# Kernel tuning notes

Measured on AMD Instinct MI355X. Metric: run time of the kernel, lower is better.

The kernel has to match this reference:

```python
import jax, jax.numpy as jnp
import numpy as np

B, N, C, H, P = 8, 4096, 256, 4, 64  # batch, tokens, hidden, heads, proj_size


def setup_inputs() -> dict:
    key = jax.random.key(0)
    ks = jax.random.split(key, 6)
    sc = 0.02
    x = jax.random.normal(ks[0], (B, N, C), jnp.float32)
    bank = jax.random.normal(ks[1], (B, N, C), jnp.float32)  # unused by forward, kept for fidelity
    W_qkvv = jax.random.normal(ks[2], (4 * C, C), jnp.float32) * sc  # Linear(C, 4C), no bias
    W_E = jax.random.normal(ks[3], (P, N), jnp.float32) * sc          # E = F shared Linear(N, P)
    b_E = jnp.zeros((P,), jnp.float32)
    temperature = jnp.ones((H, 1, 1), jnp.float32)
    temperature2 = jnp.ones((H, 1, 1), jnp.float32)
    W_out1 = jax.random.normal(ks[4], (C // 2, C), jnp.float32) * sc  # out_proj (spatial branch)
    b_out1 = jnp.zeros((C // 2,), jnp.float32)
    W_out2 = jax.random.normal(ks[5], (C // 2, C), jnp.float32) * sc  # out_proj2 (channel branch)
    b_out2 = jnp.zeros((C // 2,), jnp.float32)
    prelu_a = jnp.array(0.25, jnp.float32)  # nn.PReLU() default: single shared slope
    return {"x": x, "bank": bank, "W_qkvv": W_qkvv, "W_E": W_E, "b_E": b_E,
            "temperature": temperature, "temperature2": temperature2,
            "W_out1": W_out1, "b_out1": b_out1, "W_out2": W_out2, "b_out2": b_out2,
            "prelu_a": prelu_a}


def _l2norm(t):
    # torch F.normalize(dim=-1): x / max(||x||_2, eps)
    return t / jnp.maximum(jnp.linalg.norm(t, axis=-1, keepdims=True), 1e-12)


def reference(x, bank, W_qkvv, W_E, b_E, temperature, temperature2,
              W_out1, b_out1, W_out2, b_out2, prelu_a):
    Bb, Nn, Cc = x.shape
    Hh = temperature.shape[0]
    d = Cc // Hh
    # qkvv projection -> [4, B, H, N, d], then transpose token/feature axes -> [B, H, d, N]
    qkvv = (x @ W_qkvv.T).reshape(Bb, Nn, 4, Hh, d).transpose(2, 0, 3, 1, 4)
    q, k, v_ca, v_sa = (qkvv[0].transpose(0, 1, 3, 2), qkvv[1].transpose(0, 1, 3, 2),
                        qkvv[2].transpose(0, 1, 3, 2), qkvv[3].transpose(0, 1, 3, 2))
    # shared linear E=F projects the token axis N -> P (applied to UNnormalized k, v_sa)
    k_proj = jnp.einsum('bhdn,pn->bhdp', k, W_E) + b_E      # [B,H,d,P]
    v_sa_proj = jnp.einsum('bhdn,pn->bhdp', v_sa, W_E) + b_E  # [B,H,d,P]
    qn = _l2norm(q)
    kn = _l2norm(k)
    # channel attention: [B,H,d,d]
    attn_ca = jax.nn.softmax(jnp.einsum('bhdn,bhen->bhde', qn, kn) * temperature, axis=-1)
    x_ca = jnp.einsum('bhde,bhen->bhdn', attn_ca, v_ca).transpose(0, 3, 1, 2).reshape(Bb, Nn, Cc)
    # spatial attention (projected): [B,H,N,P]
    attn_sa = jax.nn.softmax(jnp.einsum('bhdn,bhdp->bhnp', qn, k_proj) * temperature2, axis=-1)
    x_sa = jnp.einsum('bhnp,bhdp->bhnd', attn_sa, v_sa_proj).transpose(0, 2, 1, 3).reshape(Bb, Nn, Cc)
    x_sa = x_sa @ W_out1.T + b_out1
    x_ca = x_ca @ W_out2.T + b_out2
    out = jnp.concatenate([x_sa, x_ca], axis=-1)
    return jnp.where(out >= 0, out, prelu_a * out)  # PReLU
```

## Files before the change

### kernel.cpp

```cpp
#include <hip/hip_runtime.h>
#include <cstdint>
#include <cstddef>

constexpr int B_ = 8, N_ = 4096, C_ = 256, H_ = 4, D_ = 64, P_ = 64;
constexpr int OC_ = 4 * C_;
constexpr int M_  = B_ * N_;
constexpr int GX_ROWS = 320;
constexpr int KS_G = 8;
constexpr int XT_TILES = M_ / 64;

#define DEV_INLINE __device__ __forceinline__

typedef unsigned short ushort_t;
typedef __attribute__((ext_vector_type(8))) short short8;
typedef __attribute__((ext_vector_type(4))) short short4v;
typedef __attribute__((ext_vector_type(4))) float floatx4;

DEV_INLINE short f2bf(float f) {
  unsigned int u = __builtin_bit_cast(unsigned int, f);
  u += 0x7FFFu + ((u >> 16) & 1u);
  return (short)(u >> 16);
}
DEV_INLINE float bf2f(ushort_t u) {
  return __builtin_bit_cast(float, (unsigned int)u << 16);
}
DEV_INLINE short4v cvt4(float4 v) {
  short4v s = {f2bf(v.x), f2bf(v.y), f2bf(v.z), f2bf(v.w)};
  return s;
}

__global__ __launch_bounds__(256) void k_cast(const float* __restrict__ x,
                                              const float* __restrict__ Wq,
                                              const float* __restrict__ WE,
                                              const float* __restrict__ W1,
                                              const float* __restrict__ W2,
                                              ushort_t* __restrict__ xb,
                                              ushort_t* __restrict__ xt,
                                              ushort_t* __restrict__ wqb,
                                              ushort_t* __restrict__ web,
                                              ushort_t* __restrict__ w1b,
                                              ushort_t* __restrict__ w2b) {
  const int t = threadIdx.x;
  if (blockIdx.x >= XT_TILES) {
    constexpr size_t WQ4 = (size_t)OC_ * C_ / 4;
    constexpr size_t WE4 = (size_t)P_ * N_ / 4;
    constexpr size_t W14 = (size_t)128 * C_ / 4;
    constexpr size_t TOTW4 = WQ4 + WE4 + 2 * W14;
    const size_t stride = (size_t)128 * 256;
    for (size_t i = (size_t)(blockIdx.x - XT_TILES) * 256 + t; i < TOTW4; i += stride) {
      const float* src; ushort_t* dst; size_t o;
      if (i < WQ4) { src = Wq; dst = wqb; o = i; }
      else if (i < WQ4 + WE4) { src = WE; dst = web; o = i - WQ4; }
      else if (i < WQ4 + WE4 + W14) { src = W1; dst = w1b; o = i - WQ4 - WE4; }
      else { src = W2; dst = w2b; o = i - WQ4 - WE4 - W14; }
      float4 v = ((const float4*)src)[o];
      *(short4v*)&dst[o * 4] = cvt4(v);
    }
    return;
  }
  __shared__ __align__(16) short Xs[64 * 264];
  const int n0 = blockIdx.x * 64;
  const int b = n0 >> 12, nl = n0 & 4095;
#pragma unroll
  for (int rep = 0; rep < 16; ++rep) {
    const int f4 = rep * 256 + t;
    const int row = f4 >> 6, c4 = f4 & 63;
    float4 v = *(const float4*)&x[(size_t)(n0 + row) * 256 + c4 * 4];
    short4v s = cvt4(v);
    *(short4v*)&xb[(size_t)(n0 + row) * 256 + c4 * 4] = s;
    *(short4v*)&Xs[row * 264 + c4 * 4] = s;
  }
  __syncthreads();
  const int ch = t;
  ushort_t* dst = &xt[((size_t)b * 256 + ch) * 4096 + nl];
#pragma unroll
  for (int g = 0; g < 8; ++g) {
    short8 o;
#pragma unroll
    for (int i = 0; i < 8; ++i) o[i] = Xs[(g * 8 + i) * 264 + ch];
    *(short8*)&dst[g * 8] = o;
  }
}

__global__ __launch_bounds__(512) void k_qv(const ushort_t* __restrict__ xb,
                                            const ushort_t* __restrict__ wqb,
                                            ushort_t* __restrict__ qv) {
  __shared__ __align__(16) short As[128 * 72];
  __shared__ __align__(16) short Bs[256 * 72];
  const int bm = blockIdx.x * 128;
  const int y = blockIdx.y;
  const int wrow = y ? 512 : 0;
  const int t = threadIdx.x;
  const int oc = t & 7, rr = t >> 3;
  const int lane = t & 63, wave = t >> 6;
  const int m16 = lane & 15, quad = lane >> 4;
  const int wm = (wave >> 2) << 6, wn = (wave & 3) << 6;
  floatx4 acc[4][4];
#pragma unroll
  for (int i = 0; i < 4; ++i)
#pragma unroll
    for (int j = 0; j < 4; ++j) acc[i][j] = (floatx4)(0.f);
#pragma unroll 1
  for (int k0 = 0; k0 < 256; k0 += 64) {
    short8 a8[2], b8[4];
#pragma unroll
    for (int rp = 0; rp < 2; ++rp)
      a8[rp] = *(const short8*)&xb[(size_t)(bm + rr + 64 * rp) * 256 + k0 + 8 * oc];
#pragma unroll
    for (int rp = 0; rp < 4; ++rp)
      b8[rp] = *(const short8*)&wqb[(size_t)(wrow + rr + 64 * rp) * 256 + k0 + 8 * oc];
    __syncthreads();
#pragma unroll
    for (int rp = 0; rp < 2; ++rp)
      *(short8*)&As[(rr + 64 * rp) * 72 + 8 * oc] = a8[rp];
#pragma unroll
    for (int rp = 0; rp < 4; ++rp)
      *(short8*)&Bs[(rr + 64 * rp) * 72 + 8 * oc] = b8[rp];
    __syncthreads();
#pragma unroll
    for (int ks = 0; ks < 2; ++ks) {
      short8 af[4], bf[4];
#pragma unroll
      for (int i = 0; i < 4; ++i)
        af[i] = *(const short8*)&As[(wm + i * 16 + m16) * 72 + ks * 32 + quad * 8];
#pragma unroll
      for (int j = 0; j < 4; ++j)
        bf[j] = *(const short8*)&Bs[(wn + j * 16 + m16) * 72 + ks * 32 + quad * 8];
#pragma unroll
      for (int i = 0; i < 4; ++i)
#pragma unroll
        for (int j = 0; j < 4; ++j)
          acc[i][j] = __builtin_amdgcn_mfma_f32_16x16x32_bf16(af[i], bf[j], acc[i][j], 0, 0, 0);
    }
  }
#pragma unroll
  for (int i = 0; i < 4; ++i)
#pragma unroll
    for (int r = 0; r < 4; ++r) {
      const int gr = bm + wm + i * 16 + quad * 4 + r;
#pragma unroll
      for (int j = 0; j < 4; ++j)
        qv[(size_t)gr * 512 + y * 256 + wn + j * 16 + m16] =
            (ushort_t)f2bf(acc[i][j][r]);
    }
}

__global__ __launch_bounds__(512) void k_gram(const ushort_t* __restrict__ xt,
                                              const ushort_t* __restrict__ web,
                                              float* __restrict__ Gxp) {
  __shared__ __align__(16) short As[128 * 72];
  __shared__ __align__(16) short Bs[256 * 72];
  const int job = blockIdx.x;
  const int y = blockIdx.y;
  const int b = y >> 3, ksp = y & 7;
  const int t = threadIdx.x;
  const int oc = t & 7, rr = t >> 3;
  const int lane = t & 63, wave = t >> 6;
  const int m16 = lane & 15, quad = lane >> 4;
  const int wm = (wave >> 2) << 6, wn = (wave & 3) << 6;
  const ushort_t* Asrc = (job < 2)
      ? xt + (size_t)(b * 256 + job * 128) * 4096 : web;
  const ushort_t* Bsrc = xt + (size_t)b * 256 * 4096;
  floatx4 acc[4][4];
#pragma unroll
  for (int i = 0; i < 4; ++i)
#pragma unroll
    for (int j = 0; j < 4; ++j) acc[i][j] = (floatx4)(0.f);
#pragma unroll 1
  for (int it = 0; it < 8; ++it) {
    const int n0 = ksp * 512 + it * 64;
    short8 a8[2], b8[4];
#pragma unroll
    for (int rp = 0; rp < 2; ++rp) {
      int ar = rr + 64 * rp;
      if (job == 2) ar &= 63;
      a8[rp] = *(const short8*)&Asrc[(size_t)ar * 4096 + n0 + 8 * oc];
    }
#pragma unroll
    for (int rp = 0; rp < 4; ++rp)
      b8[rp] = *(const short8*)&Bsrc[(size_t)(rr + 64 * rp) * 4096 + n0 + 8 * oc];
    __syncthreads();
#pragma unroll
    for (int rp = 0; rp < 2; ++rp)
      *(short8*)&As[(rr + 64 * rp) * 72 + 8 * oc] = a8[rp];
#pragma unroll
    for (int rp = 0; rp < 4; ++rp)
      *(short8*)&Bs[(rr + 64 * rp) * 72 + 8 * oc] = b8[rp];
    __syncthreads();
#pragma unroll
    for (int ks = 0; ks < 2; ++ks) {
      if (job < 2) {
        short8 af[4], bf[4];
#pragma unroll
        for (int i = 0; i < 4; ++i)
          af[i] = *(const short8*)&As[(wm + i * 16 + m16) * 72 + ks * 32 + quad * 8];
#pragma unroll
        for (int j = 0; j < 4; ++j)
          bf[j] = *(const short8*)&Bs[(wn + j * 16 + m16) * 72 + ks * 32 + quad * 8];
#pragma unroll
        for (int i = 0; i < 4; ++i)
#pragma unroll
          for (int j = 0; j < 4; ++j)
            acc[i][j] = __builtin_amdgcn_mfma_f32_16x16x32_bf16(af[i], bf[j], acc[i][j], 0, 0, 0);
      } else {
        short8 af[4], bf[2];
#pragma unroll
        for (int i = 0; i < 4; ++i)
          af[i] = *(const short8*)&As[(i * 16 + m16) * 72 + ks * 32 + quad * 8];
#pragma unroll
        for (int j = 0; j < 2; ++j)
          bf[j] = *(const short8*)&Bs[(wave * 32 + j * 16 + m16) * 72 + ks * 32 + quad * 8];
#pragma unroll
        for (int i = 0; i < 4; ++i)
#pragma unroll
          for (int j = 0; j < 2; ++j)
            acc[i][j] = __builtin_amdgcn_mfma_f32_16x16x32_bf16(af[i], bf[j], acc[i][j], 0, 0, 0);
      }
    }
  }
  float* pb = Gxp + (size_t)y * (GX_ROWS * 256);
  if (job < 2) {
#pragma unroll
    for (int i = 0; i < 4; ++i)
#pragma unroll
      for (int r = 0; r < 4; ++r) {
        const int grow = job * 128 + wm + i * 16 + quad * 4 + r;
#pragma unroll
        for (int j = 0; j < 4; ++j)
          pb[(size_t)grow * 256 + wn + j * 16 + m16] = acc[i][j][r];
      }
  } else {
#pragma unroll
    for (int i = 0; i < 4; ++i)
#pragma unroll
      for (int r = 0; r < 4; ++r) {
        const int grow = 256 + i * 16 + quad * 4 + r;
#pragma unroll
        for (int j = 0; j < 2; ++j)
          pb[(size_t)grow * 256 + wave * 32 + j * 16 + m16] = acc[i][j][r];
      }
  }
}

__global__ __launch_bounds__(256) void k_gred(const float* __restrict__ Gxp,
                                              float* __restrict__ Gx) {
  const int i = blockIdx.x * 256 + threadIdx.x;
  constexpr int PB4 = GX_ROWS * 256 / 4;
  const int fb = i / PB4, rem = i - fb * PB4;
  const float4* p = (const float4*)Gxp;
  float4 s = p[(size_t)fb * KS_G * PB4 + rem];
#pragma unroll
  for (int k = 1; k < KS_G; ++k) {
    float4 v = p[((size_t)fb * KS_G + k) * PB4 + rem];
    s.x += v.x; s.y += v.y; s.z += v.z; s.w += v.w;
  }
  ((float4*)Gx)[i] = s;
}

__global__ __launch_bounds__(256) void k_mid1(const ushort_t* __restrict__ wqb,
                                              const float* __restrict__ Gx,
                                              ushort_t* __restrict__ T2b,
                                              float* __restrict__ ssq) {
  __shared__ __align__(16) short As[128 * 72];
  __shared__ __align__(16) short Bs[128 * 72];
  const int bm = blockIdx.x * 128;
  const int b  = blockIdx.y >> 1;
  const int jb = blockIdx.y & 1;
  const int t = threadIdx.x;
  const int oc = t & 7;
  const int rr = t >> 3;
  const int lane = t & 63, wave = t >> 6;
  const int m16 = lane & 15, quad = lane >> 4;
  const int wm = (wave >> 1) << 6, wn = (wave & 1) << 6;
  const float* Bsrc = Gx + ((size_t)b * GX_ROWS + jb * 128) * 256;
  floatx4 acc[4][4];
#pragma unroll
  for (int i = 0; i < 4; ++i)
#pragma unroll
    for (int j = 0; j < 4; ++j) acc[i][j] = (floatx4)(0.f);
#pragma unroll 1
  for (int k0 = 0; k0 < 256; k0 += 64) {
    short8 a8[4], b8[4];
#pragma unroll
    for (int j = 0; j < 4; ++j) {
      const int r = rr + 32 * j;
      a8[j] = *(const short8*)&wqb[(size_t)(bm + r) * 256 + k0 + 8 * oc];
      float4 g0 = *(const float4*)&Bsrc[(size_t)r * 256 + k0 + 8 * oc];
      float4 g1 = *(const float4*)&Bsrc[(size_t)r * 256 + k0 + 8 * oc + 4];
      short8 bb;
      bb[0] = f2bf(g0.x); bb[1] = f2bf(g0.y); bb[2] = f2bf(g0.z); bb[3] = f2bf(g0.w);
      bb[4] = f2bf(g1.x); bb[5] = f2bf(g1.y); bb[6] = f2bf(g1.z); bb[7] = f2bf(g1.w);
      b8[j] = bb;
    }
    __syncthreads();
#pragma unroll
    for (int j = 0; j < 4; ++j) {
      const int r = rr + 32 * j;
      *(short8*)&As[r * 72 + 8 * oc] = a8[j];
      *(short8*)&Bs[r * 72 + 8 * oc] = b8[j];
    }
    __syncthreads();
#pragma unroll
    for (int ks = 0; ks < 2; ++ks) {
      short8 af[4], bf[4];
#pragma unroll
      for (int i = 0; i < 4; ++i)
        af[i] = *(const short8*)&As[(wm + i * 16 + m16) * 72 + ks * 32 + quad * 8];
#pragma unroll
      for (int j = 0; j < 4; ++j)
        bf[j] = *(const short8*)&Bs[(wn + j * 16 + m16) * 72 + ks * 32 + quad * 8];
#pragma unroll
      for (int i = 0; i < 4; ++i)
#pragma unroll
        for (int j = 0; j < 4; ++j)
          acc[i][j] = __builtin_amdgcn_mfma_f32_16x16x32_bf16(af[i], bf[j], acc[i][j], 0, 0, 0);
    }
  }
#pragma unroll
  for (int i = 0; i < 4; ++i)
#pragma unroll
    for (int r = 0; r < 4; ++r) {
      const int gr = bm + wm + i * 16 + quad * 4 + r;
      float s = 0.f;
#pragma unroll
      for (int j = 0; j < 4; ++j) {
        const int col = jb * 128 + wn + j * 16 + m16;
        T2b[((size_t)b * 512 + gr) * 256 + col] = (ushort_t)f2bf(acc[i][j][r]);
        s += bf2f(wqb[(size_t)gr * 256 + col]) * acc[i][j][r];
      }
      s += __shfl_xor(s, 1);
      s += __shfl_xor(s, 2);
      s += __shfl_xor(s, 4);
      s += __shfl_xor(s, 8);
      if (m16 == 0) atomicAdd(&ssq[b * 512 + gr], s);
    }
}

__global__ __launch_bounds__(256) void k_mid2(const ushort_t* __restrict__ wqb,
                                              const ushort_t* __restrict__ T2b,
                                              const float* __restrict__ Gx,
                                              const float* __restrict__ ssq,
                                              const float* __restrict__ bE,
                                              const float* __restrict__ t1,
                                              const float* __restrict__ t2,
                                              ushort_t* __restrict__ ab,
                                              ushort_t* __restrict__ ksb,
                                              ushort_t* __restrict__ vsb) {
  const int bh = blockIdx.x;
  const int job = blockIdx.y;
  const int b = bh >> 2, h = bh & 3;
  const int wave = threadIdx.x >> 6;
  const int lane = threadIdx.x & 63;
  const int m16 = lane & 15, quad = lane >> 4;
  const int Abase = (job == 0 ? 0 : (job == 1 ? 256 : 768)) + h * 64;
  const int arow = Abase + 16 * wave + m16;
  floatx4 acc[4];
#pragma unroll
  for (int j = 0; j < 4; ++j) acc[j] = (floatx4)(0.f);
#pragma unroll
  for (int ks = 0; ks < 8; ++ks) {
    const int boct = ks * 32 + quad * 8;
    short8 af = *(const short8*)&wqb[(size_t)arow * 256 + boct];
    short8 bf[4];
    if (job == 0) {
#pragma unroll
      for (int j = 0; j < 4; ++j)
        bf[j] = *(const short8*)&T2b[((size_t)b * 512 + 256 + h * 64 + 16 * j + m16) * 256 + boct];
    } else {
#pragma unroll
      for (int j = 0; j < 4; ++j) {
        const float* gp = Gx + ((size_t)b * GX_ROWS + 256 + 16 * j + m16) * 256 + boct;
        float4 g0 = *(const float4*)gp;
        float4 g1 = *(const float4*)(gp + 4);
        short8 bb;
        bb[0] = f2bf(g0.x); bb[1] = f2bf(g0.y); bb[2] = f2bf(g0.z); bb[3] = f2bf(g0.w);
        bb[4] = f2bf(g1.x); bb[5] = f2bf(g1.y); bb[6] = f2bf(g1.z); bb[7] = f2bf(g1.w);
        bf[j] = bb;
      }
    }
#pragma unroll
    for (int j = 0; j < 4; ++j)
      acc[j] = __builtin_amdgcn_mfma_f32_16x16x32_bf16(af, bf[j], acc[j], 0, 0, 0);
  }
  if (job == 0) {
    const float t1h = t1[h];
    float rnk[4];
#pragma unroll
    for (int j = 0; j < 4; ++j)
      rnk[j] = 1.f / fmaxf(sqrtf(ssq[b * 512 + 256 + h * 64 + 16 * j + m16]), 1e-12f);
#pragma unroll
    for (int r = 0; r < 4; ++r) {
      const int d = 16 * wave + quad * 4 + r;
      const float rq = 1.f / fmaxf(sqrtf(ssq[b * 512 + h * 64 + d]), 1e-12f);
      float l[4];
      float m = -1e30f;
#pragma unroll
      for (int j = 0; j < 4; ++j) {
        l[j] = acc[j][r] * rq * rnk[j] * t1h;
        m = fmaxf(m, l[j]);
      }
      m = fmaxf(m, __shfl_xor(m, 1));
      m = fmaxf(m, __shfl_xor(m, 2));
      m = fmaxf(m, __shfl_xor(m, 4));
      m = fmaxf(m, __shfl_xor(m, 8));
      float s = 0.f;
#pragma unroll
      for (int j = 0; j < 4; ++j) {
        l[j] = __expf(l[j] - m);
        s += l[j];
      }
      s += __shfl_xor(s, 1);
      s += __shfl_xor(s, 2);
      s += __shfl_xor(s, 4);
      s += __shfl_xor(s, 8);
      const float inv = 1.f / s;
#pragma unroll
      for (int j = 0; j < 4; ++j)
        ab[(size_t)bh * 4096 + d * 64 + 16 * j + m16] = (ushort_t)f2bf(l[j] * inv);
    }
  } else if (job == 1) {
    const float tt = t2[h];
#pragma unroll
    for (int r = 0; r < 4; ++r) {
      const int d = 16 * wave + quad * 4 + r;
      const float rq = 1.f / fmaxf(sqrtf(ssq[b * 512 + h * 64 + d]), 1e-12f);
#pragma unroll
      for (int j = 0; j < 4; ++j) {
        const int p = 16 * j + m16;
        ksb[(size_t)bh * 4096 + p * 64 + d] =
            (ushort_t)f2bf((acc[j][r] + bE[p]) * rq * tt);
      }
    }
  } else {
#pragma unroll
    for (int r = 0; r < 4; ++r) {
      const int d = 16 * wave + quad * 4 + r;
#pragma unroll
      for (int j = 0; j < 4; ++j) {
        const int p = 16 * j + m16;
        vsb[(size_t)bh * 4096 + d * 64 + p] = (ushort_t)f2bf(acc[j][r] + bE[p]);
      }
    }
  }
}

__global__ __launch_bounds__(256) void k_attn(const ushort_t* __restrict__ qv,
                                              const ushort_t* __restrict__ ab,
                                              const ushort_t* __restrict__ ksb,
                                              const ushort_t* __restrict__ vsb,
                                              ushort_t* __restrict__ x_ca,
                                              ushort_t* __restrict__ x_sa) {
  __shared__ float Pl[64][68];
  const int bh = blockIdx.x;
  const int b = bh >> 2, h = bh & 3;
  const int lane = threadIdx.x & 63, wave = threadIdx.x >> 6;
  const int m16 = lane & 15, quad = lane >> 4;
  if (blockIdx.y < 32) {
    const int n0 = blockIdx.y * 128;
    const ushort_t* abb = ab + (size_t)bh * 4096;
    short8 bf[2][4];
#pragma unroll
    for (int ks = 0; ks < 2; ++ks)
#pragma unroll
      for (int j = 0; j < 4; ++j)
        bf[ks][j] = *(const short8*)&abb[(16 * j + m16) * 64 + ks * 32 + quad * 8];
#pragma unroll
    for (int mm = 0; mm < 2; ++mm) {
      const int tokbase = n0 + 64 * mm + 16 * wave;
      const ushort_t* vrow =
          qv + (size_t)(b * N_ + tokbase + m16) * 512 + 256 + h * 64 + quad * 8;
      short8 af0 = *(const short8*)&vrow[0];
      short8 af1 = *(const short8*)&vrow[32];
      floatx4 o[4];
#pragma unroll
      for (int j = 0; j < 4; ++j) o[j] = (floatx4)(0.f);
#pragma unroll
      for (int j = 0; j < 4; ++j) {
        o[j] = __builtin_amdgcn_mfma_f32_16x16x32_bf16(af0, bf[0][j], o[j], 0, 0, 0);
        o[j] = __builtin_amdgcn_mfma_f32_16x16x32_bf16(af1, bf[1][j], o[j], 0, 0, 0);
      }
#pragma unroll
      for (int j = 0; j < 4; ++j)
#pragma unroll
        for (int r = 0; r < 4; ++r)
          x_ca[(size_t)(b * N_ + tokbase + quad * 4 + r) * C_ + h * 64 + 16 * j + m16] =
              (ushort_t)f2bf(o[j][r]);
    }
    return;
  }
  const int n0 = (blockIdx.y - 32) * 64;
  const ushort_t* qrow =
      qv + (size_t)(b * N_ + n0 + 16 * wave + m16) * 512 + h * 64 + quad * 8;
  short8 qf0 = *(const short8*)&qrow[0];
  short8 qf1 = *(const short8*)&qrow[32];
  const ushort_t* kb = ksb + (size_t)bh * 4096;
  const ushort_t* vb = vsb + (size_t)bh * 4096;
  short8 kf[2][4], vf[2][4];
#pragma unroll
  for (int ks = 0; ks < 2; ++ks)
#pragma unroll
    for (int j = 0; j < 4; ++j) {
      kf[ks][j] = *(const short8*)&kb[(16 * j + m16) * 64 + ks * 32 + quad * 8];
      vf[ks][j] = *(const short8*)&vb[(16 * j + m16) * 64 + ks * 32 + quad * 8];
    }
  floatx4 s[4];
#pragma unroll
  for (int j = 0; j < 4; ++j) s[j] = (floatx4)(0.f);
#pragma unroll
  for (int j = 0; j < 4; ++j) {
    s[j] = __builtin_amdgcn_mfma_f32_16x16x32_bf16(qf0, kf[0][j], s[j], 0, 0, 0);
    s[j] = __builtin_amdgcn_mfma_f32_16x16x32_bf16(qf1, kf[1][j], s[j], 0, 0, 0);
  }
  float p[4][4];
#pragma unroll
  for (int r = 0; r < 4; ++r) {
    float mr = fmaxf(fmaxf(s[0][r], s[1][r]), fmaxf(s[2][r], s[3][r]));
    mr = fmaxf(mr, __shfl_xor(mr, 1));
    mr = fmaxf(mr, __shfl_xor(mr, 2));
    mr = fmaxf(mr, __shfl_xor(mr, 4));
    mr = fmaxf(mr, __shfl_xor(mr, 8));
    float sr = 0.f;
#pragma unroll
    for (int j = 0; j < 4; ++j) {
      const float e = __expf(s[j][r] - mr);
      p[j][r] = e;
      sr += e;
    }
    sr += __shfl_xor(sr, 1);
    sr += __shfl_xor(sr, 2);
    sr += __shfl_xor(sr, 4);
    sr += __shfl_xor(sr, 8);
    const float inv = 1.f / sr;
#pragma unroll
    for (int j = 0; j < 4; ++j) p[j][r] *= inv;
  }
#pragma unroll
  for (int j = 0; j < 4; ++j)
#pragma unroll
    for (int r = 0; r < 4; ++r)
      Pl[16 * wave + quad * 4 + r][16 * j + m16] = p[j][r];
  __syncthreads();
  short8 pf[2];
#pragma unroll
  for (int ks = 0; ks < 2; ++ks) {
    float4 x0 = *(const float4*)&Pl[16 * wave + m16][ks * 32 + quad * 8];
    float4 x1 = *(const float4*)&Pl[16 * wave + m16][ks * 32 + quad * 8 + 4];
    short8 v;
    v[0] = f2bf(x0.x); v[1] = f2bf(x0.y); v[2] = f2bf(x0.z); v[3] = f2bf(x0.w);
    v[4] = f2bf(x1.x); v[5] = f2bf(x1.y); v[6] = f2bf(x1.z); v[7] = f2bf(x1.w);
    pf[ks] = v;
  }
  floatx4 o[4];
#pragma unroll
  for (int j = 0; j < 4; ++j) o[j] = (floatx4)(0.f);
#pragma unroll
  for (int j = 0; j < 4; ++j) {
    o[j] = __builtin_amdgcn_mfma_f32_16x16x32_bf16(pf[0], vf[0][j], o[j], 0, 0, 0);
    o[j] = __builtin_amdgcn_mfma_f32_16x16x32_bf16(pf[1], vf[1][j], o[j], 0, 0, 0);
  }
#pragma unroll
  for (int j = 0; j < 4; ++j)
#pragma unroll
    for (int r = 0; r < 4; ++r)
      x_sa[(size_t)(b * N_ + n0 + 16 * wave + quad * 4 + r) * C_ + h * 64 + 16 * j + m16] =
          (ushort_t)f2bf(o[j][r]);
}

__global__ __launch_bounds__(256) void k_out_mfma(const ushort_t* __restrict__ xsa,
                                                  const ushort_t* __restrict__ xca,
                                                  const ushort_t* __restrict__ w1b,
                                                  const float* __restrict__ b1,
                                                  const ushort_t* __restrict__ w2b,
                                                  const float* __restrict__ b2,
                                                  const float* __restrict__ pa,
                                                  float* __restrict__ out) {
  __shared__ __align__(16) short As[128 * 72];
  __shared__ __align__(16) short Bs[128 * 72];
  const int bm = blockIdx.x * 128;
  const int half = blockIdx.y;
  const ushort_t* A = half ? xca : xsa;
  const ushort_t* W = half ? w2b : w1b;
  const float* bias = half ? b2 : b1;
  const int t = threadIdx.x;
  const int oc = t & 7;
  const int rr = t >> 3;
  const int lane = t & 63, wave = t >> 6;
  const int m16 = lane & 15, quad = lane >> 4;
  const int wm = (wave >> 1) << 6, wn = (wave & 1) << 6;
  floatx4 acc[4][4];
#pragma unroll
  for (int i = 0; i < 4; ++i)
#pragma unroll
    for (int j = 0; j < 4; ++j) acc[i][j] = (floatx4)(0.f);
#pragma unroll 1
  for (int k0 = 0; k0 < 256; k0 += 64) {
    short8 a8[4], b8[4];
#pragma unroll
    for (int j = 0; j < 4; ++j) {
      const int r = rr + 32 * j;
      a8[j] = *(const short8*)&A[(size_t)(bm + r) * 256 + k0 + 8 * oc];
      b8[j] = *(const short8*)&W[(size_t)r * 256 + k0 + 8 * oc];
    }
    __syncthreads();
#pragma unroll
    for (int j = 0; j < 4; ++j) {
      const int r = rr + 32 * j;
      *(short8*)&As[r * 72 + 8 * oc] = a8[j];
      *(short8*)&Bs[r * 72 + 8 * oc] = b8[j];
    }
    __syncthreads();
#pragma unroll
    for (int ks = 0; ks < 2; ++ks) {
      short8 af[4], bf[4];
#pragma unroll
      for (int i = 0; i < 4; ++i)
        af[i] = *(const short8*)&As[(wm + i * 16 + m16) * 72 + ks * 32 + quad * 8];
#pragma unroll
      for (int j = 0; j < 4; ++j)
        bf[j] = *(const short8*)&Bs[(wn + j * 16 + m16) * 72 + ks * 32 + quad * 8];
#pragma unroll
      for (int i = 0; i < 4; ++i)
#pragma unroll
        for (int j = 0; j < 4; ++j)
          acc[i][j] = __builtin_amdgcn_mfma_f32_16x16x32_bf16(af[i], bf[j], acc[i][j], 0, 0, 0);
    }
  }
  const float slope = pa[0];
  float bj[4];
#pragma unroll
  for (int j = 0; j < 4; ++j) bj[j] = bias[wn + j * 16 + m16];
#pragma unroll
  for (int i = 0; i < 4; ++i)
#pragma unroll
    for (int r = 0; r < 4; ++r) {
      const int gr = bm + wm + i * 16 + quad * 4 + r;
#pragma unroll
      for (int j = 0; j < 4; ++j) {
        float v = acc[i][j][r] + bj[j];
        v = v >= 0.f ? v : slope * v;
        out[(size_t)gr * C_ + half * 128 + wn + j * 16 + m16] = v;
      }
    }
}

extern "C" void kernel_launch(void* const* d_in, const int* in_sizes, int n_in,
                              void* d_out, int out_size, void* d_ws, size_t ws_size,
                              hipStream_t stream) {
  (void)in_sizes; (void)n_in; (void)out_size; (void)ws_size;
  const float* x  = (const float*)d_in[0];
  const float* Wq = (const float*)d_in[2];
  const float* WE = (const float*)d_in[3];
  const float* bE = (const float*)d_in[4];
  const float* t1 = (const float*)d_in[5];
  const float* t2 = (const float*)d_in[6];
  const float* W1 = (const float*)d_in[7];
  const float* b1 = (const float*)d_in[8];
  const float* W2 = (const float*)d_in[9];
  const float* b2 = (const float*)d_in[10];
  const float* pa = (const float*)d_in[11];
  float* out = (float*)d_out;

  float* ws = (float*)d_ws;
  size_t off = 0;
  float* Gx  = ws + off; off += (size_t)B_ * GX_ROWS * 256;
  float* ssq = ws + off; off += (size_t)B_ * 512;
  float* Gxp = ws + off; off += (size_t)KS_G * B_ * GX_ROWS * 256;
  ushort_t* qv  = (ushort_t*)(ws + off); off += (size_t)M_ * 512 / 2;
  ushort_t* xsa = (ushort_t*)(ws + off); off += (size_t)M_ * C_ / 2;
  ushort_t* xca = (ushort_t*)(ws + off); off += (size_t)M_ * C_ / 2;
  ushort_t* ksb = (ushort_t*)(ws + off); off += 32 * 4096 / 2;
  ushort_t* vsb = (ushort_t*)(ws + off); off += 32 * 4096 / 2;
  ushort_t* ab  = (ushort_t*)(ws + off); off += 32 * 4096 / 2;
  ushort_t* xb  = (ushort_t*)(ws + off); off += (size_t)M_ * C_ / 2;
  ushort_t* xt  = (ushort_t*)(ws + off); off += (size_t)M_ * C_ / 2;
  ushort_t* wqb = (ushort_t*)(ws + off); off += (size_t)OC_ * C_ / 2;
  ushort_t* w1b = (ushort_t*)(ws + off); off += (size_t)128 * C_ / 2;
  ushort_t* w2b = (ushort_t*)(ws + off); off += (size_t)128 * C_ / 2;
  ushort_t* web = (ushort_t*)(ws + off); off += (size_t)P_ * N_ / 2;
  ushort_t* T2b = (ushort_t*)(ws + off); off += (size_t)B_ * 512 * C_ / 2;

  hipMemsetAsync(ssq, 0, (size_t)B_ * 512 * sizeof(float), stream);

  k_cast<<<XT_TILES + 128, 256, 0, stream>>>(x, Wq, WE, W1, W2,
                                             xb, xt, wqb, web, w1b, w2b);
  k_qv<<<dim3(M_ / 128, 2), 512, 0, stream>>>(xb, wqb, qv);
  k_gram<<<dim3(3, B_ * KS_G), 512, 0, stream>>>(xt, web, Gxp);
  k_gred<<<GX_ROWS * 256 * B_ / 4 / 256, 256, 0, stream>>>(Gxp, Gx);
  k_mid1<<<dim3(4, B_ * 2), 256, 0, stream>>>(wqb, Gx, T2b, ssq);
  k_mid2<<<dim3(32, 3), 256, 0, stream>>>(wqb, T2b, Gx, ssq, bE, t1, t2, ab, ksb, vsb);
  k_attn<<<dim3(32, 96), 256, 0, stream>>>(qv, ab, ksb, vsb, xca, xsa);
  k_out_mfma<<<dim3(M_ / 128, 2), 256, 0, stream>>>(xsa, xca, w1b, b1, w2b, b2, pa, out);
}
```

Measured before the change: 237.6 us.

## Fuse q/v projection, attention and output projection into one per-token-tile kernel

Replaces the separate q/v projection GEMM, the attention kernel and the output projection kernel with a single kernel that works on 64-token tiles. It converts x to bf16 in shared memory, computes q and v_ca for all heads, applies spatial softmax attention and channel attention per head (one wave per head), then runs both output projections with PReLU directly from LDS. This removes the global round trips for qv, x_sa, x_ca and xb and two launches. In exchange each block uses about 100KB of LDS and reads weight fragments straight from global/L2 without staging, which may limit occupancy and reload weights once per tile.

```diff
diff --git a/kernel.cpp b/kernel.cpp
--- a/kernel.cpp
+++ b/kernel.cpp
@@ -34,7 +34,6 @@
                                               const float* __restrict__ WE,
                                               const float* __restrict__ W1,
                                               const float* __restrict__ W2,
-                                              ushort_t* __restrict__ xb,
                                               ushort_t* __restrict__ xt,
                                               ushort_t* __restrict__ wqb,
                                               ushort_t* __restrict__ web,
@@ -66,9 +65,7 @@
     const int f4 = rep * 256 + t;
     const int row = f4 >> 6, c4 = f4 & 63;
     float4 v = *(const float4*)&x[(size_t)(n0 + row) * 256 + c4 * 4];
-    short4v s = cvt4(v);
-    *(short4v*)&xb[(size_t)(n0 + row) * 256 + c4 * 4] = s;
-    *(short4v*)&Xs[row * 264 + c4 * 4] = s;
+    *(short4v*)&Xs[row * 264 + c4 * 4] = cvt4(v);
   }
   __syncthreads();
   const int ch = t;
@@ -80,69 +77,6 @@
     for (int i = 0; i < 8; ++i) o[i] = Xs[(g * 8 + i) * 264 + ch];
     *(short8*)&dst[g * 8] = o;
   }
-}
-
-__global__ __launch_bounds__(512) void k_qv(const ushort_t* __restrict__ xb,
-                                            const ushort_t* __restrict__ wqb,
-                                            ushort_t* __restrict__ qv) {
-  __shared__ __align__(16) short As[128 * 72];
-  __shared__ __align__(16) short Bs[256 * 72];
-  const int bm = blockIdx.x * 128;
-  const int y = blockIdx.y;
-  const int wrow = y ? 512 : 0;
-  const int t = threadIdx.x;
-  const int oc = t & 7, rr = t >> 3;
-  const int lane = t & 63, wave = t >> 6;
-  const int m16 = lane & 15, quad = lane >> 4;
-  const int wm = (wave >> 2) << 6, wn = (wave & 3) << 6;
-  floatx4 acc[4][4];
-#pragma unroll
-  for (int i = 0; i < 4; ++i)
-#pragma unroll
-    for (int j = 0; j < 4; ++j) acc[i][j] = (floatx4)(0.f);
-#pragma unroll 1
-  for (int k0 = 0; k0 < 256; k0 += 64) {
-    short8 a8[2], b8[4];
-#pragma unroll
-    for (int rp = 0; rp < 2; ++rp)
-      a8[rp] = *(const short8*)&xb[(size_t)(bm + rr + 64 * rp) * 256 + k0 + 8 * oc];
-#pragma unroll
-    for (int rp = 0; rp < 4; ++rp)
-      b8[rp] = *(const short8*)&wqb[(size_t)(wrow + rr + 64 * rp) * 256 + k0 + 8 * oc];
-    __syncthreads();
-#pragma unroll
-    for (int rp = 0; rp < 2; ++rp)
-      *(short8*)&As[(rr + 64 * rp) * 72 + 8 * oc] = a8[rp];
-#pragma unroll
-    for (int rp = 0; rp < 4; ++rp)
-      *(short8*)&Bs[(rr + 64 * rp) * 72 + 8 * oc] = b8[rp];
-    __syncthreads();
-#pragma unroll
-    for (int ks = 0; ks < 2; ++ks) {
-      short8 af[4], bf[4];
-#pragma unroll
-      for (int i = 0; i < 4; ++i)
-        af[i] = *(const short8*)&As[(wm + i * 16 + m16) * 72 + ks * 32 + quad * 8];
-#pragma unroll
-      for (int j = 0; j < 4; ++j)
-        bf[j] = *(const short8*)&Bs[(wn + j * 16 + m16) * 72 + ks * 32 + quad * 8];
-#pragma unroll
-      for (int i = 0; i < 4; ++i)
-#pragma unroll
-        for (int j = 0; j < 4; ++j)
-          acc[i][j] = __builtin_amdgcn_mfma_f32_16x16x32_bf16(af[i], bf[j], acc[i][j], 0, 0, 0);
-    }
-  }
-#pragma unroll
-  for (int i = 0; i < 4; ++i)
-#pragma unroll
-    for (int r = 0; r < 4; ++r) {
-      const int gr = bm + wm + i * 16 + quad * 4 + r;
-#pragma unroll
-      for (int j = 0; j < 4; ++j)
-        qv[(size_t)gr * 512 + y * 256 + wn + j * 16 + m16] =
-            (ushort_t)f2bf(acc[i][j][r]);
-    }
 }
 
 __global__ __launch_bounds__(512) void k_gram(const ushort_t* __restrict__ xt,
@@ -444,203 +378,230 @@
   }
 }
 
-__global__ __launch_bounds__(256) void k_attn(const ushort_t* __restrict__ qv,
-                                              const ushort_t* __restrict__ ab,
-                                              const ushort_t* __restrict__ ksb,
-                                              const ushort_t* __restrict__ vsb,
-                                              ushort_t* __restrict__ x_ca,
-                                              ushort_t* __restrict__ x_sa) {
-  __shared__ float Pl[64][68];
-  const int bh = blockIdx.x;
-  const int b = bh >> 2, h = bh & 3;
-  const int lane = threadIdx.x & 63, wave = threadIdx.x >> 6;
-  const int m16 = lane & 15, quad = lane >> 4;
-  if (blockIdx.y < 32) {
-    const int n0 = blockIdx.y * 128;
-    const ushort_t* abb = ab + (size_t)bh * 4096;
-    short8 bf[2][4];
-#pragma unroll
-    for (int ks = 0; ks < 2; ++ks)
-#pragma unroll
-      for (int j = 0; j < 4; ++j)
-        bf[ks][j] = *(const short8*)&abb[(16 * j + m16) * 64 + ks * 32 + quad * 8];
-#pragma unroll
-    for (int mm = 0; mm < 2; ++mm) {
-      const int tokbase = n0 + 64 * mm + 16 * wave;
-      const ushort_t* vrow =
-          qv + (size_t)(b * N_ + tokbase + m16) * 512 + 256 + h * 64 + quad * 8;
-      short8 af0 = *(const short8*)&vrow[0];
-      short8 af1 = *(const short8*)&vrow[32];
-      floatx4 o[4];
-#pragma unroll
-      for (int j = 0; j < 4; ++j) o[j] = (floatx4)(0.f);
-#pragma unroll
-      for (int j = 0; j < 4; ++j) {
-        o[j] = __builtin_amdgcn_mfma_f32_16x16x32_bf16(af0, bf[0][j], o[j], 0, 0, 0);
-        o[j] = __builtin_amdgcn_mfma_f32_16x16x32_bf16(af1, bf[1][j], o[j], 0, 0, 0);
-      }
-#pragma unroll
-      for (int j = 0; j < 4; ++j)
-#pragma unroll
-        for (int r = 0; r < 4; ++r)
-          x_ca[(size_t)(b * N_ + tokbase + quad * 4 + r) * C_ + h * 64 + 16 * j + m16] =
-              (ushort_t)f2bf(o[j][r]);
-    }
-    return;
-  }
-  const int n0 = (blockIdx.y - 32) * 64;
-  const ushort_t* qrow =
-      qv + (size_t)(b * N_ + n0 + 16 * wave + m16) * 512 + h * 64 + quad * 8;
-  short8 qf0 = *(const short8*)&qrow[0];
-  short8 qf1 = *(const short8*)&qrow[32];
-  const ushort_t* kb = ksb + (size_t)bh * 4096;
-  const ushort_t* vb = vsb + (size_t)bh * 4096;
-  short8 kf[2][4], vf[2][4];
-#pragma unroll
-  for (int ks = 0; ks < 2; ++ks)
-#pragma unroll
-    for (int j = 0; j < 4; ++j) {
-      kf[ks][j] = *(const short8*)&kb[(16 * j + m16) * 64 + ks * 32 + quad * 8];
-      vf[ks][j] = *(const short8*)&vb[(16 * j + m16) * 64 + ks * 32 + quad * 8];
-    }
-  floatx4 s[4];
-#pragma unroll
-  for (int j = 0; j < 4; ++j) s[j] = (floatx4)(0.f);
-#pragma unroll
-  for (int j = 0; j < 4; ++j) {
-    s[j] = __builtin_amdgcn_mfma_f32_16x16x32_bf16(qf0, kf[0][j], s[j], 0, 0, 0);
-    s[j] = __builtin_amdgcn_mfma_f32_16x16x32_bf16(qf1, kf[1][j], s[j], 0, 0, 0);
-  }
-  float p[4][4];
-#pragma unroll
-  for (int r = 0; r < 4; ++r) {
-    float mr = fmaxf(fmaxf(s[0][r], s[1][r]), fmaxf(s[2][r], s[3][r]));
-    mr = fmaxf(mr, __shfl_xor(mr, 1));
-    mr = fmaxf(mr, __shfl_xor(mr, 2));
-    mr = fmaxf(mr, __shfl_xor(mr, 4));
-    mr = fmaxf(mr, __shfl_xor(mr, 8));
-    float sr = 0.f;
-#pragma unroll
-    for (int j = 0; j < 4; ++j) {
-      const float e = __expf(s[j][r] - mr);
-      p[j][r] = e;
-      sr += e;
-    }
-    sr += __shfl_xor(sr, 1);
-    sr += __shfl_xor(sr, 2);
-    sr += __shfl_xor(sr, 4);
-    sr += __shfl_xor(sr, 8);
-    const float inv = 1.f / sr;
-#pragma unroll
-    for (int j = 0; j < 4; ++j) p[j][r] *= inv;
-  }
-#pragma unroll
-  for (int j = 0; j < 4; ++j)
-#pragma unroll
-    for (int r = 0; r < 4; ++r)
-      Pl[16 * wave + quad * 4 + r][16 * j + m16] = p[j][r];
-  __syncthreads();
-  short8 pf[2];
-#pragma unroll
-  for (int ks = 0; ks < 2; ++ks) {
-    float4 x0 = *(const float4*)&Pl[16 * wave + m16][ks * 32 + quad * 8];
-    float4 x1 = *(const float4*)&Pl[16 * wave + m16][ks * 32 + quad * 8 + 4];
-    short8 v;
-    v[0] = f2bf(x0.x); v[1] = f2bf(x0.y); v[2] = f2bf(x0.z); v[3] = f2bf(x0.w);
-    v[4] = f2bf(x1.x); v[5] = f2bf(x1.y); v[6] = f2bf(x1.z); v[7] = f2bf(x1.w);
-    pf[ks] = v;
-  }
-  floatx4 o[4];
-#pragma unroll
-  for (int j = 0; j < 4; ++j) o[j] = (floatx4)(0.f);
-#pragma unroll
-  for (int j = 0; j < 4; ++j) {
-    o[j] = __builtin_amdgcn_mfma_f32_16x16x32_bf16(pf[0], vf[0][j], o[j], 0, 0, 0);
-    o[j] = __builtin_amdgcn_mfma_f32_16x16x32_bf16(pf[1], vf[1][j], o[j], 0, 0, 0);
-  }
-#pragma unroll
-  for (int j = 0; j < 4; ++j)
-#pragma unroll
-    for (int r = 0; r < 4; ++r)
-      x_sa[(size_t)(b * N_ + n0 + 16 * wave + quad * 4 + r) * C_ + h * 64 + 16 * j + m16] =
-          (ushort_t)f2bf(o[j][r]);
-}
-
-__global__ __launch_bounds__(256) void k_out_mfma(const ushort_t* __restrict__ xsa,
-                                                  const ushort_t* __restrict__ xca,
-                                                  const ushort_t* __restrict__ w1b,
-                                                  const float* __restrict__ b1,
-                                                  const ushort_t* __restrict__ w2b,
-                                                  const float* __restrict__ b2,
-                                                  const float* __restrict__ pa,
-                                                  float* __restrict__ out) {
-  __shared__ __align__(16) short As[128 * 72];
-  __shared__ __align__(16) short Bs[128 * 72];
-  const int bm = blockIdx.x * 128;
-  const int half = blockIdx.y;
-  const ushort_t* A = half ? xca : xsa;
-  const ushort_t* W = half ? w2b : w1b;
-  const float* bias = half ? b2 : b1;
+__global__ __launch_bounds__(256) void k_tok(const float* __restrict__ x,
+                                             const ushort_t* __restrict__ wqb,
+                                             const ushort_t* __restrict__ ab,
+                                             const ushort_t* __restrict__ ksb,
+                                             const ushort_t* __restrict__ vsb,
+                                             const ushort_t* __restrict__ w1b,
+                                             const float* __restrict__ b1,
+                                             const ushort_t* __restrict__ w2b,
+                                             const float* __restrict__ b2,
+                                             const float* __restrict__ pa,
+                                             float* __restrict__ out) {
+  __shared__ __align__(16) short Xs[64 * 264];
+  __shared__ __align__(16) short Qs[64 * 264];
+  __shared__ __align__(16) short Vs[64 * 264];
+  const int n0 = blockIdx.x * 64;
+  const int b = n0 >> 12;
   const int t = threadIdx.x;
-  const int oc = t & 7;
-  const int rr = t >> 3;
   const int lane = t & 63, wave = t >> 6;
   const int m16 = lane & 15, quad = lane >> 4;
-  const int wm = (wave >> 1) << 6, wn = (wave & 1) << 6;
-  floatx4 acc[4][4];
-#pragma unroll
-  for (int i = 0; i < 4; ++i)
-#pragma unroll
-    for (int j = 0; j < 4; ++j) acc[i][j] = (floatx4)(0.f);
+  const int cw = wave * 64;
+#pragma unroll
+  for (int rep = 0; rep < 16; ++rep) {
+    const int f4 = rep * 256 + t;
+    const int row = f4 >> 6, c4 = f4 & 63;
+    float4 v = *(const float4*)&x[(size_t)(n0 + row) * 256 + c4 * 4];
+    *(short4v*)&Xs[row * 264 + c4 * 4] = cvt4(v);
+  }
+  __syncthreads();
 #pragma unroll 1
-  for (int k0 = 0; k0 < 256; k0 += 64) {
-    short8 a8[4], b8[4];
-#pragma unroll
-    for (int j = 0; j < 4; ++j) {
-      const int r = rr + 32 * j;
-      a8[j] = *(const short8*)&A[(size_t)(bm + r) * 256 + k0 + 8 * oc];
-      b8[j] = *(const short8*)&W[(size_t)r * 256 + k0 + 8 * oc];
-    }
-    __syncthreads();
-#pragma unroll
-    for (int j = 0; j < 4; ++j) {
-      const int r = rr + 32 * j;
-      *(short8*)&As[r * 72 + 8 * oc] = a8[j];
-      *(short8*)&Bs[r * 72 + 8 * oc] = b8[j];
-    }
-    __syncthreads();
+  for (int pass = 0; pass < 2; ++pass) {
+    const int wrow = (pass ? 512 : 0) + cw;
+    short* dst = pass ? Vs : Qs;
+    floatx4 acc[4][4];
+#pragma unroll
+    for (int i = 0; i < 4; ++i)
+#pragma unroll
+      for (int j = 0; j < 4; ++j) acc[i][j] = (floatx4)(0.f);
+#pragma unroll
+    for (int ks = 0; ks < 8; ++ks) {
+      const int boct = ks * 32 + quad * 8;
+      short8 af[4], bf[4];
+#pragma unroll
+      for (int i = 0; i < 4; ++i)
+        af[i] = *(const short8*)&Xs[(16 * i + m16) * 264 + boct];
+#pragma unroll
+      for (int j = 0; j < 4; ++j)
+        bf[j] = *(const short8*)&wqb[(size_t)(wrow + 16 * j + m16) * 256 + boct];
+#pragma unroll
+      for (int i = 0; i < 4; ++i)
+#pragma unroll
+        for (int j = 0; j < 4; ++j)
+          acc[i][j] = __builtin_amdgcn_mfma_f32_16x16x32_bf16(af[i], bf[j], acc[i][j], 0, 0, 0);
+    }
+#pragma unroll
+    for (int i = 0; i < 4; ++i)
+#pragma unroll
+      for (int r = 0; r < 4; ++r)
+#pragma unroll
+        for (int j = 0; j < 4; ++j)
+          dst[(16 * i + quad * 4 + r) * 264 + cw + 16 * j + m16] =
+              (short)f2bf(acc[i][j][r]);
+  }
+  __syncthreads();
+  const int bh = b * 4 + wave;
+  {
+    floatx4 s[4][4];
+#pragma unroll
+    for (int i = 0; i < 4; ++i)
+#pragma unroll
+      for (int j = 0; j < 4; ++j) s[i][j] = (floatx4)(0.f);
 #pragma unroll
     for (int ks = 0; ks < 2; ++ks) {
+      const int boct = ks * 32 + quad * 8;
       short8 af[4], bf[4];
 #pragma unroll
       for (int i = 0; i < 4; ++i)
-        af[i] = *(const short8*)&As[(wm + i * 16 + m16) * 72 + ks * 32 + quad * 8];
-#pragma unroll
-      for (int j = 0; j < 4; ++j)
-        bf[j] = *(const short8*)&Bs[(wn + j * 16 + m16) * 72 + ks * 32 + quad * 8];
+        af[i] = *(const short8*)&Qs[(16 * i + m16) * 264 + cw + boct];
+#pragma unroll
+      for (int j = 0; j < 4; ++j)
+        bf[j] = *(const short8*)&ksb[(size_t)bh * 4096 + (16 * j + m16) * 64 + boct];
+#pragma unroll
+      for (int i = 0; i < 4; ++i)
+#pragma unroll
+        for (int j = 0; j < 4; ++j)
+          s[i][j] = __builtin_amdgcn_mfma_f32_16x16x32_bf16(af[i], bf[j], s[i][j], 0, 0, 0);
+    }
+#pragma unroll
+    for (int i = 0; i < 4; ++i)
+#pragma unroll
+      for (int r = 0; r < 4; ++r) {
+        float mr = fmaxf(fmaxf(s[i][0][r], s[i][1][r]), fmaxf(s[i][2][r], s[i][3][r]));
+        mr = fmaxf(mr, __shfl_xor(mr, 1));
+        mr = fmaxf(mr, __shfl_xor(mr, 2));
+        mr = fmaxf(mr, __shfl_xor(mr, 4));
+        mr = fmaxf(mr, __shfl_xor(mr, 8));
+        float sr = 0.f;
+#pragma unroll
+        for (int j = 0; j < 4; ++j) {
+          const float e = __expf(s[i][j][r] - mr);
+          s[i][j][r] = e;
+          sr += e;
+        }
+        sr += __shfl_xor(sr, 1);
+        sr += __shfl_xor(sr, 2);
+        sr += __shfl_xor(sr, 4);
+        sr += __shfl_xor(sr, 8);
+        const float inv = 1.f / sr;
+#pragma unroll
+        for (int j = 0; j < 4; ++j) s[i][j][r] *= inv;
+      }
+#pragma unroll
+    for (int i = 0; i < 4; ++i)
+#pragma unroll
+      for (int r = 0; r < 4; ++r)
+#pragma unroll
+        for (int j = 0; j < 4; ++j)
+          Qs[(16 * i + quad * 4 + r) * 264 + cw + 16 * j + m16] =
+              (short)f2bf(s[i][j][r]);
+    floatx4 o[4][4];
+#pragma unroll
+    for (int i = 0; i < 4; ++i)
+#pragma unroll
+      for (int j = 0; j < 4; ++j) o[i][j] = (floatx4)(0.f);
+#pragma unroll
+    for (int ks = 0; ks < 2; ++ks) {
+      const int boct = ks * 32 + quad * 8;
+      short8 af[4], bf[4];
+#pragma unroll
+      for (int i = 0; i < 4; ++i)
+        af[i] = *(const short8*)&Qs[(16 * i + m16) * 264 + cw + boct];
+#pragma unroll
+      for (int j = 0; j < 4; ++j)
+        bf[j] = *(const short8*)&vsb[(size_t)bh * 4096 + (16 * j + m16) * 64 + boct];
+#pragma unroll
+      for (int i = 0; i < 4; ++i)
+#pragma unroll
+        for (int j = 0; j < 4; ++j)
+          o[i][j] = __builtin_amdgcn_mfma_f32_16x16x32_bf16(af[i], bf[j], o[i][j], 0, 0, 0);
+    }
+#pragma unroll
+    for (int i = 0; i < 4; ++i)
+#pragma unroll
+      for (int r = 0; r < 4; ++r)
+#pragma unroll
+        for (int j = 0; j < 4; ++j)
+          Xs[(16 * i + quad * 4 + r) * 264 + cw + 16 * j + m16] =
+              (short)f2bf(o[i][j][r]);
+  }
+  {
+    floatx4 o[4][4];
+#pragma unroll
+    for (int i = 0; i < 4; ++i)
+#pragma unroll
+      for (int j = 0; j < 4; ++j) o[i][j] = (floatx4)(0.f);
+#pragma unroll
+    for (int ks = 0; ks < 2; ++ks) {
+      const int boct = ks * 32 + quad * 8;
+      short8 af[4], bf[4];
+#pragma unroll
+      for (int i = 0; i < 4; ++i)
+        af[i] = *(const short8*)&Vs[(16 * i + m16) * 264 + cw + boct];
+#pragma unroll
+      for (int j = 0; j < 4; ++j)
+        bf[j] = *(const short8*)&ab[(size_t)bh * 4096 + (16 * j + m16) * 64 + boct];
+#pragma unroll
+      for (int i = 0; i < 4; ++i)
+#pragma unroll
+        for (int j = 0; j < 4; ++j)
+          o[i][j] = __builtin_amdgcn_mfma_f32_16x16x32_bf16(af[i], bf[j], o[i][j], 0, 0, 0);
+    }
+#pragma unroll
+    for (int i = 0; i < 4; ++i)
+#pragma unroll
+      for (int r = 0; r < 4; ++r)
+#pragma unroll
+        for (int j = 0; j < 4; ++j)
+          Vs[(16 * i + quad * 4 + r) * 264 + cw + 16 * j + m16] =
+              (short)f2bf(o[i][j][r]);
+  }
+  __syncthreads();
+  {
+    const short* Asrc = (wave < 2) ? Xs : Vs;
+    const ushort_t* Wsrc = (wave < 2) ? w1b : w2b;
+    const float* bias = (wave < 2) ? b1 : b2;
+    const int wrow = (wave & 1) * 64;
+    const int colbase = (wave < 2 ? 0 : 128) + wrow;
+    floatx4 acc[4][4];
+#pragma unroll
+    for (int i = 0; i < 4; ++i)
+#pragma unroll
+      for (int j = 0; j < 4; ++j) acc[i][j] = (floatx4)(0.f);
+#pragma unroll
+    for (int ks = 0; ks < 8; ++ks) {
+      const int boct = ks * 32 + quad * 8;
+      short8 af[4], bf[4];
+#pragma unroll
+      for (int i = 0; i < 4; ++i)
+        af[i] = *(const short8*)&Asrc[(16 * i + m16) * 264 + boct];
+#pragma unroll
+      for (int j = 0; j < 4; ++j)
+        bf[j] = *(const short8*)&Wsrc[(size_t)(wrow + 16 * j + m16) * 256 + boct];
 #pragma unroll
       for (int i = 0; i < 4; ++i)
 #pragma unroll
         for (int j = 0; j < 4; ++j)
           acc[i][j] = __builtin_amdgcn_mfma_f32_16x16x32_bf16(af[i], bf[j], acc[i][j], 0, 0, 0);
     }
-  }
-  const float slope = pa[0];
-  float bj[4];
-#pragma unroll
-  for (int j = 0; j < 4; ++j) bj[j] = bias[wn + j * 16 + m16];
-#pragma unroll
-  for (int i = 0; i < 4; ++i)
-#pragma unroll
-    for (int r = 0; r < 4; ++r) {
-      const int gr = bm + wm + i * 16 + quad * 4 + r;
-#pragma unroll
-      for (int j = 0; j < 4; ++j) {
-        float v = acc[i][j][r] + bj[j];
-        v = v >= 0.f ? v : slope * v;
-        out[(size_t)gr * C_ + half * 128 + wn + j * 16 + m16] = v;
-      }
-    }
+    const float slope = pa[0];
+    float bj[4];
+#pragma unroll
+    for (int j = 0; j < 4; ++j) bj[j] = bias[wrow + 16 * j + m16];
+#pragma unroll
+    for (int i = 0; i < 4; ++i)
+#pragma unroll
+      for (int r = 0; r < 4; ++r) {
+        const int gr = n0 + 16 * i + quad * 4 + r;
+#pragma unroll
+        for (int j = 0; j < 4; ++j) {
+          float v = acc[i][j][r] + bj[j];
+          v = v >= 0.f ? v : slope * v;
+          out[(size_t)gr * C_ + colbase + 16 * j + m16] = v;
+        }
+      }
+  }
 }
 
 extern "C" void kernel_launch(void* const* d_in, const int* in_sizes, int n_in,
@@ -665,13 +626,9 @@
   float* Gx  = ws + off; off += (size_t)B_ * GX_ROWS * 256;
   float* ssq = ws + off; off += (size_t)B_ * 512;
   float* Gxp = ws + off; off += (size_t)KS_G * B_ * GX_ROWS * 256;
-  ushort_t* qv  = (ushort_t*)(ws + off); off += (size_t)M_ * 512 / 2;
-  ushort_t* xsa = (ushort_t*)(ws + off); off += (size_t)M_ * C_ / 2;
-  ushort_t* xca = (ushort_t*)(ws + off); off += (size_t)M_ * C_ / 2;
   ushort_t* ksb = (ushort_t*)(ws + off); off += 32 * 4096 / 2;
   ushort_t* vsb = (ushort_t*)(ws + off); off += 32 * 4096 / 2;
   ushort_t* ab  = (ushort_t*)(ws + off); off += 32 * 4096 / 2;
-  ushort_t* xb  = (ushort_t*)(ws + off); off += (size_t)M_ * C_ / 2;
   ushort_t* xt  = (ushort_t*)(ws + off); off += (size_t)M_ * C_ / 2;
   ushort_t* wqb = (ushort_t*)(ws + off); off += (size_t)OC_ * C_ / 2;
   ushort_t* w1b = (ushort_t*)(ws + off); off += (size_t)128 * C_ / 2;
@@ -682,12 +639,10 @@
   hipMemsetAsync(ssq, 0, (size_t)B_ * 512 * sizeof(float), stream);
 
   k_cast<<<XT_TILES + 128, 256, 0, stream>>>(x, Wq, WE, W1, W2,
-                                             xb, xt, wqb, web, w1b, w2b);
-  k_qv<<<dim3(M_ / 128, 2), 512, 0, stream>>>(xb, wqb, qv);
+                                             xt, wqb, web, w1b, w2b);
   k_gram<<<dim3(3, B_ * KS_G), 512, 0, stream>>>(xt, web, Gxp);
   k_gred<<<GX_ROWS * 256 * B_ / 4 / 256, 256, 0, stream>>>(Gxp, Gx);
   k_mid1<<<dim3(4, B_ * 2), 256, 0, stream>>>(wqb, Gx, T2b, ssq);
   k_mid2<<<dim3(32, 3), 256, 0, stream>>>(wqb, T2b, Gx, ssq, bE, t1, t2, ab, ksb, vsb);
-  k_attn<<<dim3(32, 96), 256, 0, stream>>>(qv, ab, ksb, vsb, xca, xsa);
-  k_out_mfma<<<dim3(M_ / 128, 2), 256, 0, stream>>>(xsa, xca, w1b, b1, w2b, b2, pa, out);
-}
+  k_tok<<<M_ / 64, 256, 0, stream>>>(x, wqb, ab, ksb, vsb, w1b, b1, w2b, b2, pa, out);
+}
```

New measurement: 227.5 us. -4.3%, faster.
